# Optimization experiments

Measured on AMD Instinct MI355X. Metric: run time of the kernel, lower is better.

Reference implementation:

```python
import jax, jax.numpy as jnp
import numpy as np

B, S, E, D, H, L, V = 8, 128, 512, 1024, 16, 4, 32000
DH = D // H
FF = 4 * D
SCALE = 1.0 / (DH ** 0.5)
NEG = -1e30


def _layer_norm(x, g, b, eps=1e-5):
    m = jnp.mean(x, axis=-1, keepdims=True)
    v = jnp.mean((x - m) ** 2, axis=-1, keepdims=True)
    return (x - m) / jnp.sqrt(v + eps) * g + b


def _rel_shift(x):
    # x: [q, k, b, n] -> TransformerXL relative shift
    q, k, b, n = x.shape
    xp = jnp.concatenate([jnp.zeros((q, 1, b, n), x.dtype), x], axis=1)
    xp = xp.reshape(k + 1, q, b, n)
    return xp[1:].reshape(q, k, b, n)


def setup_inputs():
    key = jax.random.key(0)
    ks = jax.random.split(key, 40)
    g = lambda i, shape, s=0.02: jax.random.normal(ks[i], shape, jnp.float32) * s
    inp = {
        'input_ids': jax.random.randint(ks[0], (B, E), 0, V),
        'encoder_rep': jax.random.normal(ks[1], (B, E, D), jnp.float32),
        'input_mask': jnp.ones((B, E), jnp.float32),
        'decode_input': jax.random.randint(ks[2], (B, S), 0, V),
        'decode_target': jax.random.randint(ks[3], (B, S), 0, V),
        'word_emb': g(4, (V, D)),
        'qkv_w': g(5, (L, 3 * D, D)), 'r_w': g(6, (L, D, D)), 'o_w': g(7, (L, D, D)),
        'kv_w': g(8, (L, 2 * D, D)), 'q_w': g(9, (L, D, D)), 'io_w': g(10, (L, D, D)),
        'rr_bias': g(11, (L, H, DH)), 'rw_bias': g(12, (L, H, DH)),
        'ln1_g': jnp.ones((L, D)), 'ln1_b': jnp.zeros((L, D)),
        'ln2_g': jnp.ones((L, D)), 'ln2_b': jnp.zeros((L, D)),
        'ffn_w1': g(13, (L, FF, D)), 'ffn_b1': jnp.zeros((L, FF)),
        'ffn_w2': g(14, (L, D, FF)), 'ffn_b2': jnp.zeros((L, D)),
        'ln3_g': jnp.ones((L, D)), 'ln3_b': jnp.zeros((L, D)),
        'out_w': g(15, (D, D)), 'out_b': jnp.zeros((D,)),
        'copy_w': g(16, (D, D)), 'copy_b': jnp.zeros((D,)),
        'mode_w': g(17, (1, D)), 'mode_b': jnp.zeros((1,)),
    }
    return inp


def _forward(input_ids, encoder_rep, input_mask, decode_input, decode_target,
             word_emb, qkv_w, r_w, o_w, kv_w, q_w, io_w, rr_bias, rw_bias,
             ln1_g, ln1_b, ln2_g, ln2_b, ffn_w1, ffn_b1, ffn_w2, ffn_b2,
             ln3_g, ln3_b, out_w, out_b, copy_w, copy_b, mode_w, mode_b):
    # relative position embedding r: [S, D]
    pos_seq = jnp.arange(S - 1, -1, -1.0, dtype=jnp.float32)
    inv_freq = 1.0 / (10000.0 ** (jnp.arange(0.0, D, 2.0) / D))
    sin_inp = pos_seq[:, None] * inv_freq[None, :]
    r = jnp.concatenate([jnp.sin(sin_inp), jnp.cos(sin_inp)], axis=-1)

    causal = jnp.tril(jnp.ones((S, S), jnp.bool_))[:, :, None, None]  # [i,j,1,1]
    enc_mask_t = input_mask.T  # [E, B]

    core = word_emb[decode_input].transpose(1, 0, 2)  # [S, B, D]
    enc_t = encoder_rep.transpose(1, 0, 2)            # [E, B, D]

    for l in range(L):
        w = core
        heads = w @ qkv_w[l].T  # [S,B,3D]
        q, k, v = jnp.split(heads, 3, axis=-1)
        q = q.reshape(S, B, H, DH); k = k.reshape(S, B, H, DH); v = v.reshape(S, B, H, DH)
        r_k = (r @ r_w[l].T).reshape(S, H, DH)
        AC = jnp.einsum('ibnd,jbnd->ijbn', q + rw_bias[l], k)
        BD = _rel_shift(jnp.einsum('ibnd,jnd->ijbn', q + rr_bias[l], r_k))
        score = (AC + BD) * SCALE
        score = jnp.where(causal, score, NEG)
        prob = jax.nn.softmax(score, axis=1)
        vec = jnp.einsum('ijbn,jbnd->ibnd', prob, v).reshape(S, B, D)
        x = _layer_norm(w + vec @ o_w[l].T, ln1_g[l], ln1_b[l])

        # cross attention
        kv = enc_t @ kv_w[l].T
        k2, v2 = jnp.split(kv, 2, axis=-1)
        k2 = k2.reshape(E, B, H, DH); v2 = v2.reshape(E, B, H, DH)
        q2 = (x @ q_w[l].T).reshape(S, B, H, DH)
        score2 = jnp.einsum('qbnd,kbnd->qkbn', q2, k2) * SCALE
        score2 = score2 + (1.0 - enc_mask_t)[None, :, :, None] * NEG
        prob2 = jax.nn.softmax(score2, axis=1)
        vec2 = jnp.einsum('ijbn,jbnd->ibnd', prob2, v2).reshape(S, B, D)
        y = _layer_norm(x + vec2 @ io_w[l].T, ln2_g[l], ln2_b[l])

        # FFN (exact GELU as torch nn.GELU default)
        h = jax.nn.gelu(y @ ffn_w1[l].T + ffn_b1[l], approximate=False)
        h = h @ ffn_w2[l].T + ffn_b2[l]
        core = _layer_norm(y + h, ln3_g[l], ln3_b[l])

    core_out = core.transpose(1, 0, 2)  # [B, S, D]
    output = core_out @ out_w.T + out_b
    vocab_logits = output @ word_emb.T  # [B,S,V]
    vocab_prob = jax.nn.softmax(vocab_logits, axis=-1)

    copy_h = core_out @ copy_w.T + copy_b
    input_logits = jnp.einsum('bid,bjd->bij', copy_h, encoder_rep)
    input_logits = input_logits + (1.0 - input_mask[:, None, :]) * NEG
    input_prob = jax.nn.softmax(input_logits, axis=-1)  # [B,S,E]

    mode_sig = jax.nn.sigmoid(core_out @ mode_w.T + mode_b)  # [B,S,1]
    vocab_prob = vocab_prob * mode_sig

    idx = jnp.broadcast_to(input_ids[:, None, :], (B, S, E))
    b_i = jnp.arange(B)[:, None, None]
    s_i = jnp.arange(S)[None, :, None]
    vocab_prob = vocab_prob.at[b_i, s_i, idx].add((1.0 - mode_sig) * input_prob)

    flat = vocab_prob.reshape(-1, V)
    tgt = decode_target.reshape(-1)
    predict = jnp.take_along_axis(flat, tgt[:, None], axis=1)[:, 0]
    valid = (tgt != 0).astype(jnp.float32)
    loss = jnp.sum(-jnp.log(predict + 1e-6) * valid) / jnp.sum(valid)
    return jnp.repeat(loss[None], B)


def reference(input_ids, encoder_rep, input_mask, decode_input, decode_target,
              word_emb, qkv_w, r_w, o_w, kv_w, q_w, io_w, rr_bias, rw_bias,
              ln1_g, ln1_b, ln2_g, ln2_b, ffn_w1, ffn_b1, ffn_w2, ffn_b2,
              ln3_g, ln3_b, out_w, out_b, copy_w, copy_b, mode_w, mode_b):
    return _forward(input_ids, encoder_rep, input_mask, decode_input, decode_target,
                    word_emb, qkv_w, r_w, o_w, kv_w, q_w, io_w, rr_bias, rw_bias,
                    ln1_g, ln1_b, ln2_g, ln2_b, ffn_w1, ffn_b1, ffn_w2, ffn_b2,
                    ln3_g, ln3_b, out_w, out_b, copy_w, copy_b, mode_w, mode_b)
```

## Files before the change

### kernel.cpp

```cpp
#include <hip/hip_runtime.h>
#include <math.h>

#define B_ 8
#define S_ 128
#define E_ 512
#define D_ 1024
#define H_ 16
#define L_ 4
#define V_ 32000
#define DH_ 64
#define FF_ 4096
#define M_ 1024
#define ME_ 4096
#define NT_ 250
#define SCALE_F 0.125f
#define NEGV (-1e30f)

typedef __attribute__((ext_vector_type(8))) short short8;
typedef __attribute__((ext_vector_type(4))) float f32x4;

__device__ __forceinline__ float bf2f(ushort u) {
  union { unsigned int u32; float f; } v; v.u32 = ((unsigned int)u) << 16; return v.f;
}
__device__ __forceinline__ ushort f2bf(float x) {
  union { float f; unsigned int u; } v; v.f = x;
  unsigned int r = v.u + 0x7fff + ((v.u >> 16) & 1);
  return (ushort)(r >> 16);
}
__device__ __forceinline__ void gl_lds16(const ushort* g, ushort* l) {
  __builtin_amdgcn_global_load_lds((const __attribute__((address_space(1))) void*)g,
                                   (__attribute__((address_space(3))) void*)l, 16, 0, 0);
}

__device__ __forceinline__ float warp_reduce_sum(float v) {
#pragma unroll
  for (int o = 32; o > 0; o >>= 1) v += __shfl_down(v, o);
  return v;
}
__device__ __forceinline__ float warp_reduce_max(float v) {
#pragma unroll
  for (int o = 32; o > 0; o >>= 1) v = fmaxf(v, __shfl_down(v, o));
  return v;
}
__device__ __forceinline__ float block_reduce_sum(float v, float* sred) {
  v = warp_reduce_sum(v);
  __syncthreads();
  if ((threadIdx.x & 63) == 0) sred[threadIdx.x >> 6] = v;
  __syncthreads();
  float s = 0.0f;
  int nw = blockDim.x >> 6;
  for (int w = 0; w < nw; ++w) s += sred[w];
  return s;
}
__device__ __forceinline__ float block_reduce_max(float v, float* sred) {
  v = warp_reduce_max(v);
  __syncthreads();
  if ((threadIdx.x & 63) == 0) sred[threadIdx.x >> 6] = v;
  __syncthreads();
  float s = -3.4e38f;
  int nw = blockDim.x >> 6;
  for (int w = 0; w < nw; ++w) s = fmaxf(s, sred[w]);
  return s;
}

__global__ __launch_bounds__(256) void castf_kernel(const float* __restrict__ in,
                                                    ushort* __restrict__ out, int n4) {
  int t = blockIdx.x * 256 + threadIdx.x;
  if (t >= n4) return;
  float4 v = ((const float4*)in)[t];
  ushort4 o;
  o.x = f2bf(v.x); o.y = f2bf(v.y); o.z = f2bf(v.z); o.w = f2bf(v.w);
  ((ushort4*)out)[t] = o;
}

__global__ __launch_bounds__(256) void enct_kernel(const float* __restrict__ enc,
                                                   ushort* __restrict__ encT) {
  int t = blockIdx.x * 256 + threadIdx.x;
  if (t >= ME_ * D_) return;
  int d = t & (D_ - 1);
  int row = t >> 10;
  int e = row >> 3, b = row & 7;
  encT[t] = f2bf(enc[((size_t)b * E_ + e) * D_ + d]);
}

__global__ __launch_bounds__(256) void pos_emb_kernel(ushort* __restrict__ r) {
  int t = blockIdx.x * 256 + threadIdx.x;
  if (t >= S_ * D_) return;
  int i = t / D_, j = t % D_;
  float pos = (float)(S_ - 1 - i);
  int jj = (j < D_ / 2) ? j : (j - D_ / 2);
  float invf = powf(10000.0f, -(float)(2 * jj) / (float)D_);
  float a = pos * invf;
  r[t] = f2bf((j < D_ / 2) ? sinf(a) : cosf(a));
}

__global__ __launch_bounds__(256) void embed_kernel(const int* __restrict__ ids,
                                                    const float* __restrict__ emb,
                                                    float* __restrict__ core,
                                                    ushort* __restrict__ core_bf) {
  int t = blockIdx.x * 256 + threadIdx.x;
  if (t >= M_ * D_) return;
  int d = t & (D_ - 1);
  int row = t >> 10;
  int s = row >> 3, b = row & 7;
  float v = emb[(size_t)ids[b * S_ + s] * D_ + d];
  core[t] = v;
  core_bf[t] = f2bf(v);
}

template <int EPI>
__global__ __launch_bounds__(256) void gemm_w_kernel(
    const ushort* __restrict__ A, const ushort* __restrict__ Bm,
    const float* __restrict__ bias, void* __restrict__ Cv,
    int M, int N, int K, int ksplit,
    long long Arow, long long Abatch, long long Brow, long long Bbatch,
    long long Crow, long long Cbatch, long long Csplit) {
  __shared__ ushort lA[128 * 32];
  __shared__ ushort lB[128 * 32];
  int tid = threadIdx.x;
  int bz = blockIdx.z;
  int batch = bz / ksplit, split = bz % ksplit;
  int kLen = K / ksplit, kStart = split * kLen;
  const ushort* Ab = A + (size_t)batch * Abatch;
  const ushort* Bb = Bm + (size_t)batch * Bbatch;
  int bm = blockIdx.y * 128, bn = blockIdx.x * 128;
  int lane = tid & 63, wave = tid >> 6;
  int wrow = (wave >> 1) * 64, wcol = (wave & 1) * 64;
  int quad = lane >> 4, l16 = lane & 15;
  f32x4 acc[4][4];
#pragma unroll
  for (int i = 0; i < 4; ++i)
#pragma unroll
    for (int j = 0; j < 4; ++j) { acc[i][j][0] = 0.f; acc[i][j][1] = 0.f; acc[i][j][2] = 0.f; acc[i][j][3] = 0.f; }
  int r0 = tid >> 2, c0 = (tid & 3) * 8;
  int r1 = (tid + 256) >> 2;
  for (int k0 = kStart; k0 < kStart + kLen; k0 += 32) {
    __syncthreads();
    gl_lds16(Ab + (size_t)(bm + r0) * Arow + k0 + c0, &lA[(size_t)tid * 8]);
    gl_lds16(Ab + (size_t)(bm + r1) * Arow + k0 + c0, &lA[(size_t)(256 + tid) * 8]);
    gl_lds16(Bb + (size_t)(bn + r0) * Brow + k0 + c0, &lB[(size_t)tid * 8]);
    gl_lds16(Bb + (size_t)(bn + r1) * Brow + k0 + c0, &lB[(size_t)(256 + tid) * 8]);
    __syncthreads();
    short8 af[4], bfr[4];
#pragma unroll
    for (int mi = 0; mi < 4; ++mi)
      af[mi] = *(const short8*)&lA[(size_t)(wrow + mi * 16 + l16) * 32 + quad * 8];
#pragma unroll
    for (int ni = 0; ni < 4; ++ni)
      bfr[ni] = *(const short8*)&lB[(size_t)(wcol + ni * 16 + l16) * 32 + quad * 8];
#pragma unroll
    for (int mi = 0; mi < 4; ++mi)
#pragma unroll
      for (int ni = 0; ni < 4; ++ni)
        acc[mi][ni] = __builtin_amdgcn_mfma_f32_16x16x32_bf16(af[mi], bfr[ni], acc[mi][ni], 0, 0, 0);
  }
#pragma unroll
  for (int mi = 0; mi < 4; ++mi) {
    int row0 = bm + wrow + mi * 16 + quad * 4;
#pragma unroll
    for (int ni = 0; ni < 4; ++ni) {
      int col = bn + wcol + ni * 16 + l16;
      float bv = 0.f;
      if (EPI >= 3) bv = bias[col];
#pragma unroll
      for (int r = 0; r < 4; ++r) {
        float v = acc[mi][ni][r] + bv;
        if (EPI == 4) v = 0.5f * v * (1.0f + erff(v * 0.70710678118654752f));
        size_t ci = (size_t)split * Csplit + (size_t)batch * Cbatch + (size_t)(row0 + r) * Crow + col;
        if (EPI == 0) ((float*)Cv)[ci] = v;
        else ((ushort*)Cv)[ci] = f2bf(v);
      }
    }
  }
}

__global__ __launch_bounds__(256) void vocab_kernel(const ushort* __restrict__ A,
                                                    const ushort* __restrict__ Bm,
                                                    float* __restrict__ tmax,
                                                    float* __restrict__ tsum) {
  __shared__ ushort lA[128 * 32];
  __shared__ ushort lB[128 * 32];
  __shared__ float smax[2][128];
  __shared__ float ssum[2][128];
  int tid = threadIdx.x;
  int bm = blockIdx.x * 128;
  int bn = blockIdx.y * 128;
  int lane = tid & 63, wave = tid >> 6;
  int wrow = (wave >> 1) * 64, half = wave & 1, wcol = half * 64;
  int quad = lane >> 4, l16 = lane & 15;
  f32x4 acc[4][4];
#pragma unroll
  for (int i = 0; i < 4; ++i)
#pragma unroll
    for (int j = 0; j < 4; ++j) { acc[i][j][0] = 0.f; acc[i][j][1] = 0.f; acc[i][j][2] = 0.f; acc[i][j][3] = 0.f; }
  int r0 = tid >> 2, c0 = (tid & 3) * 8;
  int r1 = (tid + 256) >> 2;
  for (int k0 = 0; k0 < D_; k0 += 32) {
    __syncthreads();
    gl_lds16(A + (size_t)(bm + r0) * 2048 + k0 + c0, &lA[(size_t)tid * 8]);
    gl_lds16(A + (size_t)(bm + r1) * 2048 + k0 + c0, &lA[(size_t)(256 + tid) * 8]);
    gl_lds16(Bm + (size_t)(bn + r0) * D_ + k0 + c0, &lB[(size_t)tid * 8]);
    gl_lds16(Bm + (size_t)(bn + r1) * D_ + k0 + c0, &lB[(size_t)(256 + tid) * 8]);
    __syncthreads();
    short8 af[4], bfr[4];
#pragma unroll
    for (int mi = 0; mi < 4; ++mi)
      af[mi] = *(const short8*)&lA[(size_t)(wrow + mi * 16 + l16) * 32 + quad * 8];
#pragma unroll
    for (int ni = 0; ni < 4; ++ni)
      bfr[ni] = *(const short8*)&lB[(size_t)(wcol + ni * 16 + l16) * 32 + quad * 8];
#pragma unroll
    for (int mi = 0; mi < 4; ++mi)
#pragma unroll
      for (int ni = 0; ni < 4; ++ni)
        acc[mi][ni] = __builtin_amdgcn_mfma_f32_16x16x32_bf16(af[mi], bfr[ni], acc[mi][ni], 0, 0, 0);
  }
#pragma unroll
  for (int mi = 0; mi < 4; ++mi)
#pragma unroll
    for (int r = 0; r < 4; ++r) {
      float lm = -3.4e38f;
#pragma unroll
      for (int ni = 0; ni < 4; ++ni) lm = fmaxf(lm, acc[mi][ni][r]);
#pragma unroll
      for (int o = 1; o < 16; o <<= 1) lm = fmaxf(lm, __shfl_xor(lm, o));
      if (l16 == 0) smax[half][wrow + mi * 16 + quad * 4 + r] = lm;
    }
  __syncthreads();
#pragma unroll
  for (int mi = 0; mi < 4; ++mi)
#pragma unroll
    for (int r = 0; r < 4; ++r) {
      int row = wrow + mi * 16 + quad * 4 + r;
      float m = fmaxf(smax[0][row], smax[1][row]);
      float ls = 0.f;
#pragma unroll
      for (int ni = 0; ni < 4; ++ni) ls += __expf(acc[mi][ni][r] - m);
#pragma unroll
      for (int o = 1; o < 16; o <<= 1) ls += __shfl_xor(ls, o);
      if (l16 == 0) ssum[half][row] = ls;
    }
  __syncthreads();
  if (tid < 128) {
    float m = fmaxf(smax[0][tid], smax[1][tid]);
    float s = ssum[0][tid] + ssum[1][tid];
    tmax[(size_t)(bm + tid) * NT_ + blockIdx.y] = m;
    tsum[(size_t)(bm + tid) * NT_ + blockIdx.y] = s;
  }
}

__global__ __launch_bounds__(256) void vocab_combine_kernel(const float* __restrict__ tmax,
                                                            const float* __restrict__ tsum,
                                                            float* __restrict__ rmax,
                                                            float* __restrict__ rsum) {
  __shared__ float sred[4];
  int m = blockIdx.x;
  float mx = -3.4e38f;
  for (int t = threadIdx.x; t < NT_; t += 256) mx = fmaxf(mx, tmax[(size_t)m * NT_ + t]);
  mx = block_reduce_max(mx, sred);
  float s = 0.f;
  for (int t = threadIdx.x; t < NT_; t += 256)
    s += tsum[(size_t)m * NT_ + t] * expf(tmax[(size_t)m * NT_ + t] - mx);
  s = block_reduce_sum(s, sred);
  if (threadIdx.x == 0) { rmax[m] = mx; rsum[m] = s; }
}

__global__ __launch_bounds__(256) void tlogit_kernel(const ushort* __restrict__ headout,
                                                     const ushort* __restrict__ emb,
                                                     const int* __restrict__ tgt,
                                                     float* __restrict__ tl) {
  __shared__ float sred[4];
  int m = blockIdx.x;
  int s = m >> 3, b = m & 7;
  int t = tgt[b * S_ + s];
  const ushort* a = headout + (size_t)m * 2048;
  const ushort* w = emb + (size_t)t * D_;
  float acc = 0.f;
  for (int i = threadIdx.x; i < D_; i += 256) acc += bf2f(a[i]) * bf2f(w[i]);
  acc = block_reduce_sum(acc, sred);
  if (threadIdx.x == 0) tl[m] = acc;
}

__global__ __launch_bounds__(256) void attn1_fused_kernel(const ushort* __restrict__ heads,
                                                          const ushort* __restrict__ rkproj,
                                                          const float* __restrict__ rw,
                                                          const float* __restrict__ rr,
                                                          ushort* __restrict__ attnA) {
  __shared__ float score[128][129];
  __shared__ ushort pP[128][136];
  __shared__ ushort vT[64][136];
  int bz = blockIdx.x;
  int b = bz >> 4, n = bz & 15;
  int tid = threadIdx.x, lane = tid & 63, wave = tid >> 6;
  int quad = lane >> 4, l16 = lane & 15;
  int wrow = wave * 32;

  {
    int j = tid >> 1, dbase = (tid & 1) * 32;
    const ushort* src = heads + (size_t)(j * 8 + b) * 3072 + 2048 + n * 64 + dbase;
#pragma unroll
    for (int c8 = 0; c8 < 4; ++c8) {
      short8 v8 = *(const short8*)(src + c8 * 8);
#pragma unroll
      for (int cc = 0; cc < 8; ++cc) vT[dbase + c8 * 8 + cc][j] = (ushort)v8[cc];
    }
  }

  short8 qrw[2][2], qrr[2][2];
#pragma unroll
  for (int mi = 0; mi < 2; ++mi) {
    int i = wrow + mi * 16 + l16;
    const ushort* qp = heads + (size_t)(i * 8 + b) * 3072 + n * 64;
#pragma unroll
    for (int kc = 0; kc < 2; ++kc) {
      int k0 = kc * 32 + quad * 8;
      short8 qv = *(const short8*)(qp + k0);
      short8 w, rv;
#pragma unroll
      for (int t = 0; t < 8; ++t) {
        float q = bf2f((ushort)qv[t]);
        w[t] = (short)f2bf(q + rw[n * 64 + k0 + t]);
        rv[t] = (short)f2bf(q + rr[n * 64 + k0 + t]);
      }
      qrw[mi][kc] = w; qrr[mi][kc] = rv;
    }
  }

  {
    f32x4 acc[2][8];
#pragma unroll
    for (int i = 0; i < 2; ++i)
#pragma unroll
      for (int j = 0; j < 8; ++j) { acc[i][j][0]=0.f; acc[i][j][1]=0.f; acc[i][j][2]=0.f; acc[i][j][3]=0.f; }
#pragma unroll
    for (int kc = 0; kc < 2; ++kc) {
      int k0 = kc * 32 + quad * 8;
      short8 kf[8];
#pragma unroll
      for (int ni = 0; ni < 8; ++ni) {
        int j = ni * 16 + l16;
        kf[ni] = *(const short8*)(heads + (size_t)(j * 8 + b) * 3072 + 1024 + n * 64 + k0);
      }
#pragma unroll
      for (int mi = 0; mi < 2; ++mi)
#pragma unroll
        for (int ni = 0; ni < 8; ++ni)
          acc[mi][ni] = __builtin_amdgcn_mfma_f32_16x16x32_bf16(qrw[mi][kc], kf[ni], acc[mi][ni], 0, 0, 0);
    }
#pragma unroll
    for (int mi = 0; mi < 2; ++mi)
#pragma unroll
      for (int ni = 0; ni < 8; ++ni)
#pragma unroll
        for (int r = 0; r < 4; ++r)
          score[wrow + mi * 16 + quad * 4 + r][ni * 16 + l16] = acc[mi][ni][r];
  }
  {
    f32x4 acc[2][8];
#pragma unroll
    for (int i = 0; i < 2; ++i)
#pragma unroll
      for (int j = 0; j < 8; ++j) { acc[i][j][0]=0.f; acc[i][j][1]=0.f; acc[i][j][2]=0.f; acc[i][j][3]=0.f; }
#pragma unroll
    for (int kc = 0; kc < 2; ++kc) {
      int k0 = kc * 32 + quad * 8;
      short8 rkf[8];
#pragma unroll
      for (int ni = 0; ni < 8; ++ni) {
        int jp = ni * 16 + l16;
        rkf[ni] = *(const short8*)(rkproj + (size_t)jp * 1024 + n * 64 + k0);
      }
#pragma unroll
      for (int mi = 0; mi < 2; ++mi)
#pragma unroll
        for (int ni = 0; ni < 8; ++ni)
          acc[mi][ni] = __builtin_amdgcn_mfma_f32_16x16x32_bf16(qrr[mi][kc], rkf[ni], acc[mi][ni], 0, 0, 0);
    }
#pragma unroll
    for (int mi = 0; mi < 2; ++mi)
#pragma unroll
      for (int r = 0; r < 4; ++r) {
        int i = wrow + mi * 16 + quad * 4 + r;
#pragma unroll
        for (int ni = 0; ni < 8; ++ni) {
          int jp = ni * 16 + l16;
          if (jp >= 127 - i) score[i][jp - 127 + i] += acc[mi][ni][r];
        }
      }
  }
  {
    int row = tid >> 1, halfc = (tid & 1) * 64;
    float mx = -3.4e38f;
    for (int c = halfc; c < halfc + 64; ++c) {
      float v = (c <= row) ? score[row][c] * SCALE_F : -3.4e38f;
      mx = fmaxf(mx, v);
    }
    mx = fmaxf(mx, __shfl_xor(mx, 1));
    float s = 0.f;
    for (int c = halfc; c < halfc + 64; ++c) {
      float e = (c <= row) ? __expf(score[row][c] * SCALE_F - mx) : 0.f;
      score[row][c] = e;
      s += e;
    }
    s += __shfl_xor(s, 1);
    float inv = 1.0f / s;
    for (int c = halfc; c < halfc + 64; ++c) pP[row][c] = f2bf(score[row][c] * inv);
  }
  __syncthreads();
  {
    f32x4 acc[2][4];
#pragma unroll
    for (int i = 0; i < 2; ++i)
#pragma unroll
      for (int j = 0; j < 4; ++j) { acc[i][j][0]=0.f; acc[i][j][1]=0.f; acc[i][j][2]=0.f; acc[i][j][3]=0.f; }
#pragma unroll
    for (int kc = 0; kc < 4; ++kc) {
      int k0 = kc * 32 + quad * 8;
      short8 pf[2], vf[4];
#pragma unroll
      for (int mi = 0; mi < 2; ++mi)
        pf[mi] = *(const short8*)&pP[wrow + mi * 16 + l16][k0];
#pragma unroll
      for (int ni = 0; ni < 4; ++ni)
        vf[ni] = *(const short8*)&vT[ni * 16 + l16][k0];
#pragma unroll
      for (int mi = 0; mi < 2; ++mi)
#pragma unroll
        for (int ni = 0; ni < 4; ++ni)
          acc[mi][ni] = __builtin_amdgcn_mfma_f32_16x16x32_bf16(pf[mi], vf[ni], acc[mi][ni], 0, 0, 0);
    }
#pragma unroll
    for (int mi = 0; mi < 2; ++mi)
#pragma unroll
      for (int r = 0; r < 4; ++r) {
        int i = wrow + mi * 16 + quad * 4 + r;
#pragma unroll
        for (int ni = 0; ni < 4; ++ni)
          attnA[(size_t)(i * 8 + b) * 1024 + n * 64 + ni * 16 + l16] = f2bf(acc[mi][ni][r]);
      }
  }
}

__global__ __launch_bounds__(256) void attn2_fused_kernel(const float* __restrict__ q0,
                                                          const float* __restrict__ q1,
                                                          const ushort* __restrict__ kvproj,
                                                          const float* __restrict__ mask,
                                                          ushort* __restrict__ attnA) {
  __shared__ ushort vT[64][136];
  __shared__ ushort pP[128][136];
  __shared__ float mtile[128];
  int bz = blockIdx.x;
  int b = bz >> 4, n = bz & 15;
  int tid = threadIdx.x, lane = tid & 63, wave = tid >> 6;
  int quad = lane >> 4, l16 = lane & 15;
  int wrow = wave * 32;
  short8 qf[2][2];
#pragma unroll
  for (int mi = 0; mi < 2; ++mi) {
    int i = wrow + mi * 16 + l16;
    size_t base = (size_t)(i * 8 + b) * 1024 + n * 64;
#pragma unroll
    for (int kc = 0; kc < 2; ++kc) {
      int k0 = kc * 32 + quad * 8;
      short8 v;
#pragma unroll
      for (int t = 0; t < 8; ++t) v[t] = (short)f2bf(q0[base + k0 + t] + q1[base + k0 + t]);
      qf[mi][kc] = v;
    }
  }
  float m_run[2][4], l_run[2][4];
#pragma unroll
  for (int mi = 0; mi < 2; ++mi)
#pragma unroll
    for (int r = 0; r < 4; ++r) { m_run[mi][r] = -3.0e38f; l_run[mi][r] = 0.f; }
  f32x4 accO[2][4];
#pragma unroll
  for (int i = 0; i < 2; ++i)
#pragma unroll
    for (int j = 0; j < 4; ++j) { accO[i][j][0]=0.f; accO[i][j][1]=0.f; accO[i][j][2]=0.f; accO[i][j][3]=0.f; }

  for (int et = 0; et < 4; ++et) {
    __syncthreads();
    {
      int j = tid >> 1, dbase = (tid & 1) * 32;
      int e = et * 128 + j;
      const ushort* src = kvproj + (size_t)(e * 8 + b) * 2048 + 1024 + n * 64 + dbase;
#pragma unroll
      for (int c8 = 0; c8 < 4; ++c8) {
        short8 v8 = *(const short8*)(src + c8 * 8);
#pragma unroll
        for (int cc = 0; cc < 8; ++cc) vT[dbase + c8 * 8 + cc][j] = (ushort)v8[cc];
      }
      if (tid < 128) mtile[tid] = (1.0f - mask[b * E_ + et * 128 + tid]) * NEGV;
    }
    f32x4 accS[2][8];
#pragma unroll
    for (int i = 0; i < 2; ++i)
#pragma unroll
      for (int j = 0; j < 8; ++j) { accS[i][j][0]=0.f; accS[i][j][1]=0.f; accS[i][j][2]=0.f; accS[i][j][3]=0.f; }
#pragma unroll
    for (int kc = 0; kc < 2; ++kc) {
      int k0 = kc * 32 + quad * 8;
      short8 kf[8];
#pragma unroll
      for (int ni = 0; ni < 8; ++ni) {
        int e = et * 128 + ni * 16 + l16;
        kf[ni] = *(const short8*)(kvproj + (size_t)(e * 8 + b) * 2048 + n * 64 + k0);
      }
#pragma unroll
      for (int mi = 0; mi < 2; ++mi)
#pragma unroll
        for (int ni = 0; ni < 8; ++ni)
          accS[mi][ni] = __builtin_amdgcn_mfma_f32_16x16x32_bf16(qf[mi][kc], kf[ni], accS[mi][ni], 0, 0, 0);
    }
    __syncthreads();
#pragma unroll
    for (int mi = 0; mi < 2; ++mi)
#pragma unroll
      for (int r = 0; r < 4; ++r) {
        float v[8];
        float vmax = -3.4e38f;
#pragma unroll
        for (int ni = 0; ni < 8; ++ni) {
          v[ni] = accS[mi][ni][r] * SCALE_F + mtile[ni * 16 + l16];
          vmax = fmaxf(vmax, v[ni]);
        }
#pragma unroll
        for (int o = 1; o < 16; o <<= 1) vmax = fmaxf(vmax, __shfl_xor(vmax, o));
        float mnew = fmaxf(m_run[mi][r], vmax);
        float alpha = __expf(m_run[mi][r] - mnew);
        float ls = 0.f;
        int row = wrow + mi * 16 + quad * 4 + r;
#pragma unroll
        for (int ni = 0; ni < 8; ++ni) {
          float p = __expf(v[ni] - mnew);
          ls += p;
          pP[row][ni * 16 + l16] = f2bf(p);
        }
#pragma unroll
        for (int o = 1; o < 16; o <<= 1) ls += __shfl_xor(ls, o);
        l_run[mi][r] = l_run[mi][r] * alpha + ls;
        m_run[mi][r] = mnew;
#pragma unroll
        for (int ni = 0; ni < 4; ++ni) accO[mi][ni][r] *= alpha;
      }
#pragma unroll
    for (int kc = 0; kc < 4; ++kc) {
      int k0 = kc * 32 + quad * 8;
      short8 pf[2], vf[4];
#pragma unroll
      for (int mi = 0; mi < 2; ++mi)
        pf[mi] = *(const short8*)&pP[wrow + mi * 16 + l16][k0];
#pragma unroll
      for (int ni = 0; ni < 4; ++ni)
        vf[ni] = *(const short8*)&vT[ni * 16 + l16][k0];
#pragma unroll
      for (int mi = 0; mi < 2; ++mi)
#pragma unroll
        for (int ni = 0; ni < 4; ++ni)
          accO[mi][ni] = __builtin_amdgcn_mfma_f32_16x16x32_bf16(pf[mi], vf[ni], accO[mi][ni], 0, 0, 0);
    }
  }
#pragma unroll
  for (int mi = 0; mi < 2; ++mi)
#pragma unroll
    for (int r = 0; r < 4; ++r) {
      int i = wrow + mi * 16 + quad * 4 + r;
      float inv = 1.0f / l_run[mi][r];
#pragma unroll
      for (int ni = 0; ni < 4; ++ni)
        attnA[(size_t)(i * 8 + b) * 1024 + n * 64 + ni * 16 + l16] = f2bf(accO[mi][ni][r] * inv);
    }
}

__global__ __launch_bounds__(256) void addln_kernel(const float* __restrict__ a,
                                                    const float* __restrict__ c,
                                                    int nsplit, long long cstride,
                                                    const float* __restrict__ bias,
                                                    const float* __restrict__ g,
                                                    const float* __restrict__ bb,
                                                    float* __restrict__ out,
                                                    ushort* __restrict__ out_bf) {
  __shared__ float sred[4];
  int row = blockIdx.x;
  const float* pa = a + (size_t)row * D_;
  float vals[4];
  float s = 0.f;
#pragma unroll
  for (int it = 0; it < 4; ++it) {
    int idx = threadIdx.x + it * 256;
    float v = pa[idx];
    for (int sp = 0; sp < nsplit; ++sp) v += c[(size_t)sp * cstride + (size_t)row * D_ + idx];
    if (bias) v += bias[idx];
    vals[it] = v;
    s += v;
  }
  s = block_reduce_sum(s, sred);
  float mean = s * (1.0f / D_);
  float ss = 0.f;
#pragma unroll
  for (int it = 0; it < 4; ++it) {
    float dd = vals[it] - mean;
    ss += dd * dd;
  }
  ss = block_reduce_sum(ss, sred);
  float inv = rsqrtf(ss * (1.0f / D_) + 1e-5f);
#pragma unroll
  for (int it = 0; it < 4; ++it) {
    int idx = threadIdx.x + it * 256;
    float r = (vals[it] - mean) * inv * g[idx] + bb[idx];
    out[(size_t)row * D_ + idx] = r;
    out_bf[(size_t)row * D_ + idx] = f2bf(r);
  }
}

__global__ __launch_bounds__(256) void mode_kernel(const float* __restrict__ core,
                                                   const float* __restrict__ mode_w,
                                                   const float* __restrict__ mode_b,
                                                   float* __restrict__ mode_sig) {
  __shared__ float sred[4];
  int m = blockIdx.x;
  const float* a = core + (size_t)m * D_;
  float s = 0.f;
  for (int t = threadIdx.x; t < D_; t += 256) s += a[t] * mode_w[t];
  s = block_reduce_sum(s, sred);
  if (threadIdx.x == 0) mode_sig[m] = 1.0f / (1.0f + expf(-(s + mode_b[0])));
}

__global__ __launch_bounds__(256) void final_kernel(const float* __restrict__ lg,
                                                    const int* __restrict__ ids,
                                                    const float* __restrict__ mask,
                                                    const int* __restrict__ tgt,
                                                    const float* __restrict__ mode_sig,
                                                    const float* __restrict__ tlogit,
                                                    const float* __restrict__ rmax,
                                                    const float* __restrict__ rsum,
                                                    float* __restrict__ loss_acc) {
  __shared__ float sred[4];
  int s = blockIdx.x, b = blockIdx.y;
  int m = s * B_ + b;
  size_t base = (size_t)(b * S_ + s) * E_;
  const long long LGS = (long long)B_ * S_ * E_;
  int tg = tgt[b * S_ + s];
  float lv[2];
  float mx = -3.4e38f;
#pragma unroll
  for (int it = 0; it < 2; ++it) {
    int e = threadIdx.x + it * 256;
    float raw = 0.f;
#pragma unroll
    for (int sp = 0; sp < 4; ++sp) raw += lg[sp * LGS + base + e];
    raw += (1.0f - mask[b * E_ + e]) * NEGV;
    lv[it] = raw;
    mx = fmaxf(mx, raw);
  }
  mx = block_reduce_max(mx, sred);
  float ssum = 0.f, csum = 0.f;
#pragma unroll
  for (int it = 0; it < 2; ++it) {
    int e = threadIdx.x + it * 256;
    float ev = expf(lv[it] - mx);
    ssum += ev;
    if (ids[b * E_ + e] == tg) csum += ev;
  }
  ssum = block_reduce_sum(ssum, sred);
  csum = block_reduce_sum(csum, sred);
  if (threadIdx.x == 0) {
    float copy_p = csum / ssum;
    float pv = expf(tlogit[m] - rmax[m]) / rsum[m];
    float msig = mode_sig[m];
    float predict = pv * msig + (1.0f - msig) * copy_p;
    float valid = (tg != 0) ? 1.0f : 0.0f;
    atomicAdd(&loss_acc[0], -logf(predict + 1e-6f) * valid);
    atomicAdd(&loss_acc[1], valid);
  }
}

__global__ void writeout_kernel(const float* __restrict__ loss_acc, float* __restrict__ out) {
  if (threadIdx.x < B_) out[threadIdx.x] = loss_acc[0] / loss_acc[1];
}

static void gw(hipStream_t st, int epi, const ushort* A, const ushort* B, const float* bias,
               void* C, int M, int N, int K,
               long long Ar, long long Ab, long long Br, long long Bb,
               long long Cr, long long Cb, int nb, int ksplit, long long Csplit) {
  dim3 g(N / 128, M / 128, nb * ksplit);
  switch (epi) {
    case 0: gemm_w_kernel<0><<<g, 256, 0, st>>>(A, B, bias, C, M, N, K, ksplit, Ar, Ab, Br, Bb, Cr, Cb, Csplit); break;
    case 1: gemm_w_kernel<1><<<g, 256, 0, st>>>(A, B, bias, C, M, N, K, ksplit, Ar, Ab, Br, Bb, Cr, Cb, Csplit); break;
    case 3: gemm_w_kernel<3><<<g, 256, 0, st>>>(A, B, bias, C, M, N, K, ksplit, Ar, Ab, Br, Bb, Cr, Cb, Csplit); break;
    case 4: gemm_w_kernel<4><<<g, 256, 0, st>>>(A, B, bias, C, M, N, K, ksplit, Ar, Ab, Br, Bb, Cr, Cb, Csplit); break;
  }
}
static void castTo(hipStream_t st, const float* src, ushort* dst, size_t count) {
  int n4 = (int)(count / 4);
  castf_kernel<<<(n4 + 255) / 256, 256, 0, st>>>(src, dst, n4);
}

extern "C" void kernel_launch(void* const* d_in, const int* in_sizes, int n_in,
                              void* d_out, int out_size, void* d_ws, size_t ws_size,
                              hipStream_t stream) {
  const int* input_ids = (const int*)d_in[0];
  const float* encoder_rep = (const float*)d_in[1];
  const float* input_mask = (const float*)d_in[2];
  const int* decode_input = (const int*)d_in[3];
  const int* decode_target = (const int*)d_in[4];
  const float* word_emb = (const float*)d_in[5];
  const float* qkv_w = (const float*)d_in[6];
  const float* r_w = (const float*)d_in[7];
  const float* o_w = (const float*)d_in[8];
  const float* kv_w = (const float*)d_in[9];
  const float* q_w = (const float*)d_in[10];
  const float* io_w = (const float*)d_in[11];
  const float* rr_bias = (const float*)d_in[12];
  const float* rw_bias = (const float*)d_in[13];
  const float* ln1_g = (const float*)d_in[14];
  const float* ln1_b = (const float*)d_in[15];
  const float* ln2_g = (const float*)d_in[16];
  const float* ln2_b = (const float*)d_in[17];
  const float* ffn_w1 = (const float*)d_in[18];
  const float* ffn_b1 = (const float*)d_in[19];
  const float* ffn_w2 = (const float*)d_in[20];
  const float* ffn_b2 = (const float*)d_in[21];
  const float* ln3_g = (const float*)d_in[22];
  const float* ln3_b = (const float*)d_in[23];
  const float* out_w = (const float*)d_in[24];
  const float* out_b = (const float*)d_in[25];
  const float* copy_w = (const float*)d_in[26];
  const float* copy_b = (const float*)d_in[27];
  const float* mode_w = (const float*)d_in[28];
  const float* mode_b = (const float*)d_in[29];
  float* out = (float*)d_out;

  char* base = (char*)d_ws;
  size_t off = 0;
  auto alloc = [&](size_t bytes) -> void* {
    void* p = base + off;
    off = (off + bytes + 255) & ~(size_t)255;
    return p;
  };

  ushort* wl_qkv = (ushort*)alloc((size_t)3 * D_ * D_ * 2);
  ushort* wl_r = (ushort*)alloc((size_t)D_ * D_ * 2);
  ushort* wl_o = (ushort*)alloc((size_t)D_ * D_ * 2);
  ushort* wl_kv = (ushort*)alloc((size_t)2 * D_ * D_ * 2);
  ushort* wl_q = (ushort*)alloc((size_t)D_ * D_ * 2);
  ushort* wl_io = (ushort*)alloc((size_t)D_ * D_ * 2);
  ushort* wl_f1 = (ushort*)alloc((size_t)FF_ * D_ * 2);
  ushort* wl_f2 = (ushort*)alloc((size_t)FF_ * D_ * 2);
  ushort* w_emb = (ushort*)alloc((size_t)V_ * D_ * 2);
  ushort* w_oc = (ushort*)alloc((size_t)2048 * D_ * 2);
  float* b_oc = (float*)alloc(2048 * 4);
  ushort* enc_bf = (ushort*)alloc((size_t)ME_ * D_ * 2);
  ushort* encT_bf = (ushort*)alloc((size_t)ME_ * D_ * 2);
  ushort* r_bf = (ushort*)alloc((size_t)S_ * D_ * 2);
  ushort* rkproj_bf = (ushort*)alloc((size_t)S_ * D_ * 2);
  float* f_core = (float*)alloc((size_t)M_ * D_ * 4);
  ushort* core_bf = (ushort*)alloc((size_t)M_ * D_ * 2);
  ushort* heads_bf = (ushort*)alloc((size_t)M_ * 3 * D_ * 2);
  ushort* attnA_bf = (ushort*)alloc((size_t)M_ * D_ * 2);
  float* f_tmp = (float*)alloc((size_t)4 * M_ * D_ * 4);
  float* f_x = (float*)alloc((size_t)M_ * D_ * 4);
  ushort* x_bf = (ushort*)alloc((size_t)M_ * D_ * 2);
  float* f_y = (float*)alloc((size_t)M_ * D_ * 4);
  ushort* y_bf = (ushort*)alloc((size_t)M_ * D_ * 2);
  ushort* kvproj_bf = (ushort*)alloc((size_t)ME_ * 2 * D_ * 2);
  float* f_q = (float*)alloc((size_t)2 * M_ * D_ * 4);
  ushort* ffnh_bf = (ushort*)alloc((size_t)M_ * FF_ * 2);
  ushort* headout_bf = (ushort*)alloc((size_t)M_ * 2048 * 2);
  float* f_lg = (float*)alloc((size_t)4 * B_ * S_ * E_ * 4);
  float* f_tmax = (float*)alloc((size_t)M_ * NT_ * 4);
  float* f_tsum = (float*)alloc((size_t)M_ * NT_ * 4);
  float* f_rmax = (float*)alloc(M_ * 4);
  float* f_rsum = (float*)alloc(M_ * 4);
  float* f_tlogit = (float*)alloc(M_ * 4);
  float* f_mode = (float*)alloc(M_ * 4);
  float* f_loss = (float*)alloc(64);

  castTo(stream, word_emb, w_emb, (size_t)V_ * D_);
  castTo(stream, out_w, w_oc, (size_t)D_ * D_);
  castTo(stream, copy_w, w_oc + (size_t)D_ * D_, (size_t)D_ * D_);
  hipMemcpyAsync(b_oc, out_b, D_ * 4, hipMemcpyDeviceToDevice, stream);
  hipMemcpyAsync(b_oc + D_, copy_b, D_ * 4, hipMemcpyDeviceToDevice, stream);
  castTo(stream, encoder_rep, enc_bf, (size_t)ME_ * D_);
  enct_kernel<<<(ME_ * D_) / 256, 256, 0, stream>>>(encoder_rep, encT_bf);
  pos_emb_kernel<<<(S_ * D_ + 255) / 256, 256, 0, stream>>>(r_bf);
  embed_kernel<<<(M_ * D_) / 256, 256, 0, stream>>>(decode_input, word_emb, f_core, core_bf);

  for (int l = 0; l < L_; ++l) {
    castTo(stream, qkv_w + (size_t)l * 3 * D_ * D_, wl_qkv, (size_t)3 * D_ * D_);
    castTo(stream, r_w + (size_t)l * D_ * D_, wl_r, (size_t)D_ * D_);
    castTo(stream, o_w + (size_t)l * D_ * D_, wl_o, (size_t)D_ * D_);
    castTo(stream, kv_w + (size_t)l * 2 * D_ * D_, wl_kv, (size_t)2 * D_ * D_);
    castTo(stream, q_w + (size_t)l * D_ * D_, wl_q, (size_t)D_ * D_);
    castTo(stream, io_w + (size_t)l * D_ * D_, wl_io, (size_t)D_ * D_);
    castTo(stream, ffn_w1 + (size_t)l * FF_ * D_, wl_f1, (size_t)FF_ * D_);
    castTo(stream, ffn_w2 + (size_t)l * FF_ * D_, wl_f2, (size_t)FF_ * D_);

    gw(stream, 1, core_bf, wl_qkv, nullptr, heads_bf, M_, 3 * D_, D_, D_, 0, D_, 0, 3 * D_, 0, 1, 1, 0);
    gw(stream, 1, r_bf, wl_r, nullptr, rkproj_bf, S_, D_, D_, D_, 0, D_, 0, D_, 0, 1, 1, 0);
    attn1_fused_kernel<<<B_ * H_, 256, 0, stream>>>(heads_bf, rkproj_bf,
                                                    rw_bias + (size_t)l * D_,
                                                    rr_bias + (size_t)l * D_, attnA_bf);
    gw(stream, 0, attnA_bf, wl_o, nullptr, f_tmp, M_, D_, D_, D_, 0, D_, 0, D_, 0, 1, 2,
       (long long)M_ * D_);
    addln_kernel<<<M_, 256, 0, stream>>>(f_core, f_tmp, 2, (long long)M_ * D_, nullptr,
                                         ln1_g + (size_t)l * D_, ln1_b + (size_t)l * D_, f_x, x_bf);

    gw(stream, 1, encT_bf, wl_kv, nullptr, kvproj_bf, ME_, 2 * D_, D_, D_, 0, D_, 0, 2 * D_, 0, 1, 1, 0);
    gw(stream, 0, x_bf, wl_q, nullptr, f_q, M_, D_, D_, D_, 0, D_, 0, D_, 0, 1, 2,
       (long long)M_ * D_);
    attn2_fused_kernel<<<B_ * H_, 256, 0, stream>>>(f_q, f_q + (size_t)M_ * D_, kvproj_bf,
                                                    input_mask, attnA_bf);
    gw(stream, 0, attnA_bf, wl_io, nullptr, f_tmp, M_, D_, D_, D_, 0, D_, 0, D_, 0, 1, 2,
       (long long)M_ * D_);
    addln_kernel<<<M_, 256, 0, stream>>>(f_x, f_tmp, 2, (long long)M_ * D_, nullptr,
                                         ln2_g + (size_t)l * D_, ln2_b + (size_t)l * D_, f_y, y_bf);

    gw(stream, 4, y_bf, wl_f1, ffn_b1 + (size_t)l * FF_, ffnh_bf, M_, FF_, D_, D_, 0, D_, 0, FF_, 0, 1, 1, 0);
    gw(stream, 0, ffnh_bf, wl_f2, nullptr, f_tmp, M_, D_, FF_, FF_, 0, FF_, 0, D_, 0, 1, 4,
       (long long)M_ * D_);
    addln_kernel<<<M_, 256, 0, stream>>>(f_y, f_tmp, 4, (long long)M_ * D_,
                                         ffn_b2 + (size_t)l * D_,
                                         ln3_g + (size_t)l * D_, ln3_b + (size_t)l * D_, f_core, core_bf);
  }

  gw(stream, 3, core_bf, w_oc, b_oc, headout_bf, M_, 2048, D_, D_, 0, D_, 0, 2048, 0, 1, 1, 0);
  mode_kernel<<<M_, 256, 0, stream>>>(f_core, mode_w, mode_b, f_mode);

  vocab_kernel<<<dim3(M_ / 128, V_ / 128), 256, 0, stream>>>(headout_bf, w_emb, f_tmax, f_tsum);
  vocab_combine_kernel<<<M_, 256, 0, stream>>>(f_tmax, f_tsum, f_rmax, f_rsum);
  tlogit_kernel<<<M_, 256, 0, stream>>>(headout_bf, w_emb, decode_target, f_tlogit);

  gw(stream, 0, headout_bf + D_, enc_bf, nullptr, f_lg, S_, E_, D_,
     (long long)B_ * 2048, 2048, D_, (long long)E_ * D_, E_, (long long)S_ * E_, B_, 4,
     (long long)B_ * S_ * E_);

  hipMemsetAsync(f_loss, 0, 2 * sizeof(float), stream);
  final_kernel<<<dim3(S_, B_), 256, 0, stream>>>(f_lg, input_ids, input_mask, decode_target,
                                                 f_mode, f_tlogit, f_rmax, f_rsum, f_loss);
  writeout_kernel<<<1, 64, 0, stream>>>(f_loss, out);
}
```

Baseline: 1.749 ms.

## Hoist layer-independent KV and R projections into batched GEMMs, merge weight casts

Moves the encoder KV projection and relative-position R projection out of the layer loop into single batched GEMMs over all four layers, which exposes more parallel work per launch. The per-layer weight casts are merged into one kernel launch. The vocab kernel's block index is also remapped so that blocks sharing a vocab tile run close together, aiming for better L2 reuse. The cost is extra workspace for the per-layer KV and R projection buffers.

Result: faster. 1.614 ms (-7.7%).

```diff
diff --git a/kernel.cpp b/kernel.cpp
--- a/kernel.cpp
+++ b/kernel.cpp
@@ -71,6 +71,28 @@
   ushort4 o;
   o.x = f2bf(v.x); o.y = f2bf(v.y); o.z = f2bf(v.z); o.w = f2bf(v.w);
   ((ushort4*)out)[t] = o;
+}
+
+__global__ __launch_bounds__(256) void castlayer_kernel(
+    const float* __restrict__ sqkv, const float* __restrict__ so,
+    const float* __restrict__ sq, const float* __restrict__ sio,
+    const float* __restrict__ sf1, const float* __restrict__ sf2,
+    ushort* __restrict__ dqkv, ushort* __restrict__ dov,
+    ushort* __restrict__ dq, ushort* __restrict__ dio,
+    ushort* __restrict__ df1, ushort* __restrict__ df2) {
+  int t = blockIdx.x * 256 + threadIdx.x;
+  const float* src; ushort* dst; int idx;
+  if (t < 786432)       { src = sqkv; dst = dqkv; idx = t; }
+  else if (t < 1048576) { src = so;  dst = dov; idx = t - 786432; }
+  else if (t < 1310720) { src = sq;  dst = dq;  idx = t - 1048576; }
+  else if (t < 1572864) { src = sio; dst = dio; idx = t - 1310720; }
+  else if (t < 2621440) { src = sf1; dst = df1; idx = t - 1572864; }
+  else if (t < 3670016) { src = sf2; dst = df2; idx = t - 2621440; }
+  else return;
+  float4 v = ((const float4*)src)[idx];
+  ushort4 o4;
+  o4.x = f2bf(v.x); o4.y = f2bf(v.y); o4.z = f2bf(v.z); o4.w = f2bf(v.w);
+  ((ushort4*)dst)[idx] = o4;
 }
 
 __global__ __launch_bounds__(256) void enct_kernel(const float* __restrict__ enc,
@@ -183,8 +205,11 @@
   __shared__ float smax[2][128];
   __shared__ float ssum[2][128];
   int tid = threadIdx.x;
-  int bm = blockIdx.x * 128;
-  int bn = blockIdx.y * 128;
+  int orig = blockIdx.x + gridDim.x * blockIdx.y;
+  int wg = (orig & 7) * 250 + (orig >> 3);
+  int bm = (wg & 7) * 128;
+  int bnT = wg >> 3;
+  int bn = bnT * 128;
   int lane = tid & 63, wave = tid >> 6;
   int wrow = (wave >> 1) * 64, half = wave & 1, wcol = half * 64;
   int quad = lane >> 4, l16 = lane & 15;
@@ -244,8 +269,8 @@
   if (tid < 128) {
     float m = fmaxf(smax[0][tid], smax[1][tid]);
     float s = ssum[0][tid] + ssum[1][tid];
-    tmax[(size_t)(bm + tid) * NT_ + blockIdx.y] = m;
-    tsum[(size_t)(bm + tid) * NT_ + blockIdx.y] = s;
+    tmax[(size_t)(bm + tid) * NT_ + bnT] = m;
+    tsum[(size_t)(bm + tid) * NT_ + bnT] = s;
   }
 }
 
@@ -741,20 +766,22 @@
   };
 
   ushort* wl_qkv = (ushort*)alloc((size_t)3 * D_ * D_ * 2);
-  ushort* wl_r = (ushort*)alloc((size_t)D_ * D_ * 2);
   ushort* wl_o = (ushort*)alloc((size_t)D_ * D_ * 2);
-  ushort* wl_kv = (ushort*)alloc((size_t)2 * D_ * D_ * 2);
   ushort* wl_q = (ushort*)alloc((size_t)D_ * D_ * 2);
   ushort* wl_io = (ushort*)alloc((size_t)D_ * D_ * 2);
   ushort* wl_f1 = (ushort*)alloc((size_t)FF_ * D_ * 2);
   ushort* wl_f2 = (ushort*)alloc((size_t)FF_ * D_ * 2);
+  ushort* wl_kv = (ushort*)alloc((size_t)L_ * 2 * D_ * D_ * 2);
+  ushort* wl_r = (ushort*)alloc((size_t)L_ * D_ * D_ * 2);
+  ushort* kvproj_bf = (ushort*)alloc((size_t)L_ * ME_ * 2 * D_ * 2);
+  ushort* rkproj_bf = (ushort*)alloc((size_t)L_ * S_ * D_ * 2);
+
   ushort* w_emb = (ushort*)alloc((size_t)V_ * D_ * 2);
   ushort* w_oc = (ushort*)alloc((size_t)2048 * D_ * 2);
   float* b_oc = (float*)alloc(2048 * 4);
   ushort* enc_bf = (ushort*)alloc((size_t)ME_ * D_ * 2);
   ushort* encT_bf = (ushort*)alloc((size_t)ME_ * D_ * 2);
   ushort* r_bf = (ushort*)alloc((size_t)S_ * D_ * 2);
-  ushort* rkproj_bf = (ushort*)alloc((size_t)S_ * D_ * 2);
   float* f_core = (float*)alloc((size_t)M_ * D_ * 4);
   ushort* core_bf = (ushort*)alloc((size_t)M_ * D_ * 2);
   ushort* heads_bf = (ushort*)alloc((size_t)M_ * 3 * D_ * 2);
@@ -764,7 +791,6 @@
   ushort* x_bf = (ushort*)alloc((size_t)M_ * D_ * 2);
   float* f_y = (float*)alloc((size_t)M_ * D_ * 4);
   ushort* y_bf = (ushort*)alloc((size_t)M_ * D_ * 2);
-  ushort* kvproj_bf = (ushort*)alloc((size_t)ME_ * 2 * D_ * 2);
   float* f_q = (float*)alloc((size_t)2 * M_ * D_ * 4);
   ushort* ffnh_bf = (ushort*)alloc((size_t)M_ * FF_ * 2);
   ushort* headout_bf = (ushort*)alloc((size_t)M_ * 2048 * 2);
@@ -787,19 +813,22 @@
   pos_emb_kernel<<<(S_ * D_ + 255) / 256, 256, 0, stream>>>(r_bf);
   embed_kernel<<<(M_ * D_) / 256, 256, 0, stream>>>(decode_input, word_emb, f_core, core_bf);
 
+  castTo(stream, kv_w, wl_kv, (size_t)L_ * 2 * D_ * D_);
+  castTo(stream, r_w, wl_r, (size_t)L_ * D_ * D_);
+  gw(stream, 1, encT_bf, wl_kv, nullptr, kvproj_bf, ME_, 2 * D_, D_,
+     D_, 0, D_, (long long)2 * D_ * D_, 2 * D_, (long long)ME_ * 2 * D_, L_, 1, 0);
+  gw(stream, 1, r_bf, wl_r, nullptr, rkproj_bf, S_, D_, D_,
+     D_, 0, D_, (long long)D_ * D_, D_, (long long)S_ * D_, L_, 1, 0);
+
   for (int l = 0; l < L_; ++l) {
-    castTo(stream, qkv_w + (size_t)l * 3 * D_ * D_, wl_qkv, (size_t)3 * D_ * D_);
-    castTo(stream, r_w + (size_t)l * D_ * D_, wl_r, (size_t)D_ * D_);
-    castTo(stream, o_w + (size_t)l * D_ * D_, wl_o, (size_t)D_ * D_);
-    castTo(stream, kv_w + (size_t)l * 2 * D_ * D_, wl_kv, (size_t)2 * D_ * D_);
-    castTo(stream, q_w + (size_t)l * D_ * D_, wl_q, (size_t)D_ * D_);
-    castTo(stream, io_w + (size_t)l * D_ * D_, wl_io, (size_t)D_ * D_);
-    castTo(stream, ffn_w1 + (size_t)l * FF_ * D_, wl_f1, (size_t)FF_ * D_);
-    castTo(stream, ffn_w2 + (size_t)l * FF_ * D_, wl_f2, (size_t)FF_ * D_);
+    castlayer_kernel<<<14336, 256, 0, stream>>>(
+        qkv_w + (size_t)l * 3 * D_ * D_, o_w + (size_t)l * D_ * D_,
+        q_w + (size_t)l * D_ * D_, io_w + (size_t)l * D_ * D_,
+        ffn_w1 + (size_t)l * FF_ * D_, ffn_w2 + (size_t)l * FF_ * D_,
+        wl_qkv, wl_o, wl_q, wl_io, wl_f1, wl_f2);
 
     gw(stream, 1, core_bf, wl_qkv, nullptr, heads_bf, M_, 3 * D_, D_, D_, 0, D_, 0, 3 * D_, 0, 1, 1, 0);
-    gw(stream, 1, r_bf, wl_r, nullptr, rkproj_bf, S_, D_, D_, D_, 0, D_, 0, D_, 0, 1, 1, 0);
-    attn1_fused_kernel<<<B_ * H_, 256, 0, stream>>>(heads_bf, rkproj_bf,
+    attn1_fused_kernel<<<B_ * H_, 256, 0, stream>>>(heads_bf, rkproj_bf + (size_t)l * S_ * D_,
                                                     rw_bias + (size_t)l * D_,
                                                     rr_bias + (size_t)l * D_, attnA_bf);
     gw(stream, 0, attnA_bf, wl_o, nullptr, f_tmp, M_, D_, D_, D_, 0, D_, 0, D_, 0, 1, 2,
@@ -807,10 +836,10 @@
     addln_kernel<<<M_, 256, 0, stream>>>(f_core, f_tmp, 2, (long long)M_ * D_, nullptr,
                                          ln1_g + (size_t)l * D_, ln1_b + (size_t)l * D_, f_x, x_bf);
 
-    gw(stream, 1, encT_bf, wl_kv, nullptr, kvproj_bf, ME_, 2 * D_, D_, D_, 0, D_, 0, 2 * D_, 0, 1, 1, 0);
     gw(stream, 0, x_bf, wl_q, nullptr, f_q, M_, D_, D_, D_, 0, D_, 0, D_, 0, 1, 2,
        (long long)M_ * D_);
-    attn2_fused_kernel<<<B_ * H_, 256, 0, stream>>>(f_q, f_q + (size_t)M_ * D_, kvproj_bf,
+    attn2_fused_kernel<<<B_ * H_, 256, 0, stream>>>(f_q, f_q + (size_t)M_ * D_,
+                                                    kvproj_bf + (size_t)l * ME_ * 2 * D_,
                                                     input_mask, attnA_bf);
     gw(stream, 0, attnA_bf, wl_io, nullptr, f_tmp, M_, D_, D_, D_, 0, D_, 0, D_, 0, 1, 2,
        (long long)M_ * D_);
```
